# Performance work log

Measured on AMD Instinct MI355X. Metric: run time of the kernel, lower is better.

The kernel has to match this reference:

```python
import jax, jax.numpy as jnp
import numpy as np

BUFFER_SIZE = 64  # chunk size == sliding window size


def setup_inputs() -> dict:
    key = jax.random.key(0)
    k1, k2, k3, k4 = jax.random.split(key, 4)
    B, S, dim = 4, 8192, 256
    D = dim * 2
    states = jax.random.normal(k1, (B, S, dim, 2), dtype=jnp.float32)
    # projection weights (module inits them to identity; use scaled random for a
    # non-trivial but numerically tame reference)
    Wq = jax.random.normal(k2, (D, D), dtype=jnp.float32) * 0.05
    Wk = jax.random.normal(k3, (D, D), dtype=jnp.float32) * 0.05
    Wv = jax.random.normal(k4, (D, D), dtype=jnp.float32) * 0.05
    return {"states": states, "Wq": Wq, "Wk": Wk, "Wv": Wv}


def reference(states, Wq, Wk, Wv):
    B, S, dim, _ = states.shape
    D = dim * 2
    C = BUFFER_SIZE
    assert S % C == 0 and S > 2 * C
    n = S // C  # number of chunks

    x = states.reshape(B, S, D)
    q = x @ Wq.T
    k = x @ Wk.T
    v = x @ Wv.T

    # chunk: [B, n, C, D]
    qc = q.reshape(B, n, C, D)
    kc = k.reshape(B, n, C, D)
    vc = v.reshape(B, n, C, D)

    # context for chunk i = chunk i-1 ++ chunk i  -> [B, n, 2C, D]
    zeros_blk = jnp.zeros_like(kc[:, :1])
    k_ctx = jnp.concatenate([jnp.concatenate([zeros_blk, kc[:, :-1]], axis=1), kc], axis=2)
    v_ctx = jnp.concatenate([jnp.concatenate([zeros_blk, vc[:, :-1]], axis=1), vc], axis=2)

    scale = 1.0 / jnp.sqrt(jnp.asarray(D, dtype=q.dtype))
    scores = jnp.einsum('bnqd,bnkd->bnqk', qc, k_ctx) * scale  # [B, n, C, 2C]

    # mask: query at local pos qi attends keys strictly before it (global),
    # i.e. context index j < C + qi; chunk 0 has no previous chunk (j >= C).
    qi = jnp.arange(C)[:, None]            # [C,1]
    j = jnp.arange(2 * C)[None, :]         # [1,2C]
    chunk_idx = jnp.arange(n)[:, None, None]
    mask = (j < C + qi)[None] & ((chunk_idx > 0) | (j >= C)[None])  # [n, C, 2C]

    scores = jnp.where(mask[None], scores, jnp.asarray(-1e30, scores.dtype))
    p = jax.nn.softmax(scores, axis=-1)
    # fully-masked rows (only global position 0) -> zero output
    row_valid = jnp.any(mask, axis=-1, keepdims=True)[None].astype(p.dtype)
    p = p * row_valid

    out = jnp.einsum('bnqk,bnkd->bnqd', p, v_ctx).reshape(B, S, D)
    out = out.at[:, 0, :].set(0.0)  # matches retrieved_flat[:, 0, :] = 0.0
    return out.reshape(B, S, dim, 2)
```

## Files before the change

kernel.cpp:

```cpp
#include <hip/hip_runtime.h>

#define SCALE 0.044194173824159216f

typedef _Float16 half8 __attribute__((ext_vector_type(8)));
typedef _Float16 half4 __attribute__((ext_vector_type(4)));
typedef float    f32x4 __attribute__((ext_vector_type(4)));

#define MFMA(A, B, Cc) __builtin_amdgcn_mfma_f32_16x16x32_f16((A), (B), (Cc), 0, 0, 0)

#define X16_OFF 0ull
#define Q16_OFF 33554432ull
#define K16_OFF 67108864ull
#define VT_OFF  100663296ull
#define W16_OFF 134217728ull
#define WS_NEED 135790592ull

typedef __attribute__((address_space(1))) const unsigned int glb_t;
typedef __attribute__((address_space(3))) unsigned int lds_t;

__device__ __forceinline__ void gl16(const void* g, void* l) {
  __builtin_amdgcn_global_load_lds((glb_t*)g, (lds_t*)l, 16, 0, 0);
}

__device__ __forceinline__ half8 ldf64(const _Float16* buf, int row, int colh) {
  int byte = row * 128 + (((colh) << 1) ^ ((row & 7) << 4));
  return *(const half8*)((const char*)buf + byte);
}
__device__ __forceinline__ half8 ldf128(const _Float16* buf, int row, int colh) {
  int byte = row * 256 + (((colh) << 1) ^ ((row & 7) << 4));
  return *(const half8*)((const char*)buf + byte);
}

__global__ __launch_bounds__(256)
void k0_cvt(const float* __restrict__ x, const float* __restrict__ Wq,
            const float* __restrict__ Wk, const float* __restrict__ Wv,
            _Float16* __restrict__ x16, _Float16* __restrict__ w16)
{
  const long long NX = 16777216LL;
  long long base = ((long long)blockIdx.x * 256 + threadIdx.x) * 8;
  const float* src;
  _Float16* dst;
  float sc = 1.0f;
  if (base < NX) {
    src = x + base; dst = x16 + base;
  } else {
    long long o = base - NX;
    int ws = (int)(o >> 18);
    long long oo = o & 262143LL;
    src = (ws == 0 ? Wq : (ws == 1 ? Wk : Wv)) + oo;
    dst = w16 + o;
    if (ws == 0) sc = SCALE;
  }
  const float4* p = (const float4*)src;
  float4 f0 = p[0], f1 = p[1];
  half8 v;
  v[0] = (_Float16)(f0.x * sc); v[1] = (_Float16)(f0.y * sc);
  v[2] = (_Float16)(f0.z * sc); v[3] = (_Float16)(f0.w * sc);
  v[4] = (_Float16)(f1.x * sc); v[5] = (_Float16)(f1.y * sc);
  v[6] = (_Float16)(f1.z * sc); v[7] = (_Float16)(f1.w * sc);
  *(half8*)dst = v;
}

__global__ __launch_bounds__(256)
void k1_gemm(const _Float16* __restrict__ x16, const _Float16* __restrict__ w16,
             _Float16* __restrict__ q16, _Float16* __restrict__ k16,
             _Float16* __restrict__ vT)
{
  __shared__ _Float16 xs[2][8192];
  __shared__ _Float16 wl[2][8192];

  const int id  = blockIdx.x;
  const int swz = (id & 7) * 384 + (id >> 3);
  const int ntile = swz % 12;
  const int stile = swz / 12;
  const int wsel  = ntile >> 2;
  const int tid = threadIdx.x, lane = tid & 63, w = tid >> 6;
  const int l15 = lane & 15, h = lane >> 4;
  const int wm = w >> 1, wn = w & 1;

  const _Float16* xb = x16 + (size_t)stile * 128 * 512;
  const _Float16* wb = w16 + (size_t)ntile * 128 * 512;

  int rowi[4], coli[4];
  #pragma unroll
  for (int i = 0; i < 4; ++i) {
    int unit = i * 256 + w * 64 + lane;
    int row = unit >> 3, u = unit & 7;
    rowi[i] = row;
    coli[i] = (u ^ (row & 7)) << 3;
  }

  f32x4 acc[4][4] = {};
  const bool vpath = (wsel == 2);

  #pragma unroll
  for (int i = 0; i < 4; ++i) {
    int ub = i * 256 + w * 64;
    gl16(xb + (size_t)rowi[i] * 512 + coli[i], &xs[0][ub * 8]);
    gl16(wb + (size_t)rowi[i] * 512 + coli[i], &wl[0][ub * 8]);
  }

  for (int kk = 0; kk < 8; ++kk) {
    const int cur = kk & 1;
    if (kk < 7) {
      const int nxt = cur ^ 1;
      #pragma unroll
      for (int i = 0; i < 4; ++i) {
        int ub = i * 256 + w * 64;
        gl16(xb + (size_t)rowi[i] * 512 + (kk + 1) * 64 + coli[i], &xs[nxt][ub * 8]);
        gl16(wb + (size_t)rowi[i] * 512 + (kk + 1) * 64 + coli[i], &wl[nxt][ub * 8]);
      }
      asm volatile("s_waitcnt vmcnt(8)" ::: "memory");
    } else {
      asm volatile("s_waitcnt vmcnt(0)" ::: "memory");
    }
    __builtin_amdgcn_s_barrier();
    __builtin_amdgcn_sched_barrier(0);

    #pragma unroll
    for (int ks = 0; ks < 2; ++ks) {
      half8 a[4], bf[4];
      if (!vpath) {
        #pragma unroll
        for (int mr = 0; mr < 4; ++mr) a[mr]  = ldf64(xs[cur], wm * 64 + mr * 16 + l15, ks * 32 + h * 8);
        #pragma unroll
        for (int nr = 0; nr < 4; ++nr) bf[nr] = ldf64(wl[cur], wn * 64 + nr * 16 + l15, ks * 32 + h * 8);
      } else {
        #pragma unroll
        for (int mr = 0; mr < 4; ++mr) a[mr]  = ldf64(wl[cur], wm * 64 + mr * 16 + l15, ks * 32 + h * 8);
        #pragma unroll
        for (int nr = 0; nr < 4; ++nr) bf[nr] = ldf64(xs[cur], wn * 64 + nr * 16 + l15, ks * 32 + h * 8);
      }
      #pragma unroll
      for (int mr = 0; mr < 4; ++mr)
        #pragma unroll
        for (int nr = 0; nr < 4; ++nr)
          acc[mr][nr] = MFMA(a[mr], bf[nr], acc[mr][nr]);
    }

    __builtin_amdgcn_sched_barrier(0);
    __builtin_amdgcn_s_barrier();
  }

  if (!vpath) {
    _Float16* dst = (wsel == 0) ? q16 : k16;
    const int m0 = stile * 128 + wm * 64;
    const int n0 = (ntile & 3) * 128 + wn * 64;
    #pragma unroll
    for (int mr = 0; mr < 4; ++mr)
      #pragma unroll
      for (int nr = 0; nr < 4; ++nr)
        #pragma unroll
        for (int r = 0; r < 4; ++r)
          dst[(size_t)(m0 + mr * 16 + h * 4 + r) * 512 + n0 + nr * 16 + l15] =
              (_Float16)acc[mr][nr][r];
  } else {
    const int d0 = (ntile & 3) * 128 + wm * 64;
    const int sg = stile * 128 + wn * 64;
    const int bb = sg >> 13, s0 = sg & 8191;
    _Float16* dst = vT + (size_t)bb * 512 * 8192;
    #pragma unroll
    for (int mr = 0; mr < 4; ++mr)
      #pragma unroll
      for (int nr = 0; nr < 4; ++nr)
        #pragma unroll
        for (int r = 0; r < 4; ++r)
          dst[(size_t)(d0 + mr * 16 + h * 4 + r) * 8192 + s0 + nr * 16 + l15] =
              (_Float16)acc[mr][nr][r];
  }
}

__global__ __launch_bounds__(256)
void k2_attn(const _Float16* __restrict__ q16, const _Float16* __restrict__ k16,
             const _Float16* __restrict__ vT, float* __restrict__ out)
{
  __shared__ _Float16 kj[2][128 * 64];
  __shared__ _Float16 p_lds[64 * 128];

  const int id = blockIdx.x;
  const int sz = (id & 7) * 64 + (id >> 3);
  const int b = sz >> 7, c = sz & 127;
  const int tid = threadIdx.x, lane = tid & 63, w = tid >> 6;
  const int l15 = lane & 15, h = lane >> 4;
  const int jbase = c * 64 - 64;

  const _Float16* qrow = q16 + (size_t)(b * 8192 + c * 64 + w * 16 + l15) * 512;
  half8 qa[16];
  #pragma unroll
  for (int ks = 0; ks < 16; ++ks) qa[ks] = *(const half8*)(qrow + ks * 32 + h * 8);

  const _Float16* kb = k16 + (size_t)b * 8192 * 512;

  f32x4 S[8] = {};
  {
    #pragma unroll
    for (int i = 0; i < 4; ++i) {
      int unit = i * 256 + w * 64 + lane;
      int row = unit >> 3, u = unit & 7;
      int sj = jbase + row; if (sj < 0) sj = 0;
      gl16(kb + (size_t)sj * 512 + ((u ^ (row & 7)) << 3), &kj[0][(i * 256 + w * 64) * 8]);
    }
    int cur = 0;
    for (int ee = 0; ee < 8; ++ee) {
      __syncthreads();
      if (ee < 7) {
        #pragma unroll
        for (int i = 0; i < 4; ++i) {
          int unit = i * 256 + w * 64 + lane;
          int row = unit >> 3, u = unit & 7;
          int sj = jbase + row; if (sj < 0) sj = 0;
          gl16(kb + (size_t)sj * 512 + (ee + 1) * 64 + ((u ^ (row & 7)) << 3),
               &kj[cur ^ 1][(i * 256 + w * 64) * 8]);
        }
      }
      #pragma unroll
      for (int ks = 0; ks < 2; ++ks) {
        #pragma unroll
        for (int nt = 0; nt < 8; ++nt) {
          half8 bf = ldf64(kj[cur], nt * 16 + l15, ks * 32 + h * 8);
          S[nt] = MFMA(qa[ee * 2 + ks], bf, S[nt]);
        }
      }
      cur ^= 1;
    }
  }

  #pragma unroll
  for (int jt = 0; jt < 8; ++jt) {
    int j = jt * 16 + l15;
    #pragma unroll
    for (int r = 0; r < 4; ++r) {
      int ql = w * 16 + h * 4 + r;
      bool valid = (j < 64 + ql) && ((c > 0) || (j >= 64));
      S[jt][r] = valid ? S[jt][r] : -1e30f;
    }
  }
  #pragma unroll
  for (int r = 0; r < 4; ++r) {
    float mx = -1e30f;
    #pragma unroll
    for (int jt = 0; jt < 8; ++jt) mx = fmaxf(mx, S[jt][r]);
    mx = fmaxf(mx, __shfl_xor(mx, 1));
    mx = fmaxf(mx, __shfl_xor(mx, 2));
    mx = fmaxf(mx, __shfl_xor(mx, 4));
    mx = fmaxf(mx, __shfl_xor(mx, 8));
    float sum = 0.f;
    #pragma unroll
    for (int jt = 0; jt < 8; ++jt) {
      float sv = S[jt][r];
      float pe = (sv > -1e29f) ? __expf(sv - mx) : 0.f;
      S[jt][r] = pe;
      sum += pe;
    }
    sum += __shfl_xor(sum, 1);
    sum += __shfl_xor(sum, 2);
    sum += __shfl_xor(sum, 4);
    sum += __shfl_xor(sum, 8);
    float inv = (sum > 0.f) ? (1.0f / sum) : 0.f;
    #pragma unroll
    for (int jt = 0; jt < 8; ++jt) {
      int row = w * 16 + h * 4 + r, col = jt * 16 + l15;
      _Float16 ph = (_Float16)(S[jt][r] * inv);
      *(_Float16*)((char*)p_lds + row * 256 + ((col << 1) ^ ((row & 7) << 4))) = ph;
    }
  }
  half8 pa[4];
  #pragma unroll
  for (int ks = 0; ks < 4; ++ks) {
    int row = w * 16 + l15, colh = ks * 32 + h * 8;
    pa[ks] = *(const half8*)((const char*)p_lds + row * 256 + ((colh << 1) ^ ((row & 7) << 4)));
  }

  const _Float16* vb = vT + (size_t)b * 512 * 8192;
  float* ob = out + (size_t)(b * 8192 + c * 64 + w * 16) * 512;

  __syncthreads();
  #pragma unroll
  for (int i = 0; i < 4; ++i) {
    int unit = i * 256 + w * 64 + lane;
    int row = unit >> 4, u = unit & 15;
    int u2 = (u & 8) | ((u & 7) ^ (row & 7));
    int js = jbase + u2 * 8; if (js < 0) js = 0;
    gl16(vb + (size_t)row * 8192 + js, &kj[0][(i * 256 + w * 64) * 8]);
  }
  int cur = 0;
  for (int dd = 0; dd < 8; ++dd) {
    __syncthreads();
    if (dd < 7) {
      #pragma unroll
      for (int i = 0; i < 4; ++i) {
        int unit = i * 256 + w * 64 + lane;
        int row = unit >> 4, u = unit & 15;
        int u2 = (u & 8) | ((u & 7) ^ (row & 7));
        int js = jbase + u2 * 8; if (js < 0) js = 0;
        gl16(vb + (size_t)((dd + 1) * 64 + row) * 8192 + js, &kj[cur ^ 1][(i * 256 + w * 64) * 8]);
      }
    }
    f32x4 o[4] = {};
    #pragma unroll
    for (int ks = 0; ks < 4; ++ks) {
      #pragma unroll
      for (int nr = 0; nr < 4; ++nr) {
        half8 bf = ldf128(kj[cur], nr * 16 + l15, ks * 32 + h * 8);
        o[nr] = MFMA(pa[ks], bf, o[nr]);
      }
    }
    #pragma unroll
    for (int nr = 0; nr < 4; ++nr)
      #pragma unroll
      for (int r = 0; r < 4; ++r)
        ob[(size_t)(h * 4 + r) * 512 + dd * 64 + nr * 16 + l15] = o[nr][r];
    cur ^= 1;
  }
}

__device__ __forceinline__ int swzb(int row, int colByte) {
  return colByte ^ ((row & 7) << 4);
}
__device__ __forceinline__ half8 ldw_frag(const float* __restrict__ W, int row, int e0) {
  const float4* p = reinterpret_cast<const float4*>(W + ((size_t)row << 9) + e0);
  float4 f0 = p[0];
  float4 f1 = p[1];
  half8 v;
  v[0] = (_Float16)f0.x; v[1] = (_Float16)f0.y; v[2] = (_Float16)f0.z; v[3] = (_Float16)f0.w;
  v[4] = (_Float16)f1.x; v[5] = (_Float16)f1.y; v[6] = (_Float16)f1.z; v[7] = (_Float16)f1.w;
  return v;
}
__device__ __forceinline__ half8 ldl_frag(const unsigned short* buf, int row, int col, int strideBytes) {
  int byte = row * strideBytes + swzb(row, col << 1);
  return *reinterpret_cast<const half8*>(reinterpret_cast<const char*>(buf) + byte);
}

__global__ __launch_bounds__(256, 1)
void ep_fused(const float* __restrict__ x, const float* __restrict__ Wq,
              const float* __restrict__ Wk, const float* __restrict__ Wv,
              float* __restrict__ out)
{
  __shared__ unsigned short xs[128 * 512];
  __shared__ unsigned short kv[64 * 128];
  __shared__ unsigned short pq[64 * 128];

  const int bc   = blockIdx.x;
  const int b    = bc >> 7;
  const int c    = bc & 127;
  const int tid  = threadIdx.x;
  const int lane = tid & 63;
  const int w    = tid >> 6;
  const int l15  = lane & 15;
  const int h    = lane >> 4;

  const float* xb = x + (size_t)b * (8192 * 512);
  #pragma unroll
  for (int i = 0; i < 32; ++i) {
    int unit = tid + (i << 8);
    int row  = unit >> 6;
    int e0   = (unit & 63) << 3;
    half8 v;
    if (c == 0 && row < 64) {
      #pragma unroll
      for (int t = 0; t < 8; ++t) v[t] = (_Float16)0.0f;
    } else {
      int s = c * 64 - 64 + row;
      const float4* p = reinterpret_cast<const float4*>(xb + (size_t)s * 512 + e0);
      float4 f0 = p[0], f1 = p[1];
      v[0] = (_Float16)f0.x; v[1] = (_Float16)f0.y; v[2] = (_Float16)f0.z; v[3] = (_Float16)f0.w;
      v[4] = (_Float16)f1.x; v[5] = (_Float16)f1.y; v[6] = (_Float16)f1.z; v[7] = (_Float16)f1.w;
    }
    int byte = (row << 10) + swzb(row, e0 << 1);
    *reinterpret_cast<half8*>(reinterpret_cast<char*>(xs) + byte) = v;
  }
  __syncthreads();

  f32x4 Sacc[8] = {};
  const int d0 = (w << 4) + (h << 2);

  for (int dt = 0; dt < 8; ++dt) {
    const int drow = (dt << 6) + (w << 4) + l15;

    f32x4 qa[4] = {};
    for (int ks = 0; ks < 16; ++ks) {
      half8 a = ldw_frag(Wq, drow, (ks << 5) + (h << 3));
      #pragma unroll
      for (int nt = 0; nt < 4; ++nt) {
        half8 bf = ldl_frag(xs, 64 + (nt << 4) + l15, (ks << 5) + (h << 3), 1024);
        qa[nt] = MFMA(a, bf, qa[nt]);
      }
    }
    #pragma unroll
    for (int nt = 0; nt < 4; ++nt) {
      int q = (nt << 4) + l15;
      half4 hv;
      hv[0] = (_Float16)qa[nt][0]; hv[1] = (_Float16)qa[nt][1];
      hv[2] = (_Float16)qa[nt][2]; hv[3] = (_Float16)qa[nt][3];
      *reinterpret_cast<half4*>(reinterpret_cast<char*>(pq) + q * 128 + swzb(q, d0 << 1)) = hv;
    }

    f32x4 ka[8] = {};
    for (int ks = 0; ks < 16; ++ks) {
      half8 a = ldw_frag(Wk, drow, (ks << 5) + (h << 3));
      #pragma unroll
      for (int nt = 0; nt < 8; ++nt) {
        half8 bf = ldl_frag(xs, (nt << 4) + l15, (ks << 5) + (h << 3), 1024);
        ka[nt] = MFMA(a, bf, ka[nt]);
      }
    }
    #pragma unroll
    for (int nt = 0; nt < 8; ++nt) {
      int j = (nt << 4) + l15;
      half4 hv;
      hv[0] = (_Float16)ka[nt][0]; hv[1] = (_Float16)ka[nt][1];
      hv[2] = (_Float16)ka[nt][2]; hv[3] = (_Float16)ka[nt][3];
      *reinterpret_cast<half4*>(reinterpret_cast<char*>(kv) + j * 128 + swzb(j, d0 << 1)) = hv;
    }
    __syncthreads();

    #pragma unroll
    for (int ksd = 0; ksd < 2; ++ksd) {
      half8 a = ldl_frag(pq, (w << 4) + l15, (ksd << 5) + (h << 3), 128);
      #pragma unroll
      for (int nt = 0; nt < 8; ++nt) {
        half8 bf = ldl_frag(kv, (nt << 4) + l15, (ksd << 5) + (h << 3), 128);
        Sacc[nt] = MFMA(a, bf, Sacc[nt]);
      }
    }
    __syncthreads();
  }

  const float scale = SCALE;
  #pragma unroll
  for (int nt = 0; nt < 8; ++nt) {
    int j = (nt << 4) + l15;
    #pragma unroll
    for (int r = 0; r < 4; ++r) {
      int qrow = (w << 4) + (h << 2) + r;
      bool valid = (j < 64 + qrow) && ((c > 0) || (j >= 64));
      Sacc[nt][r] = valid ? Sacc[nt][r] * scale : -1e30f;
    }
  }
  float inv[4];
  #pragma unroll
  for (int r = 0; r < 4; ++r) {
    float mx = -1e30f;
    #pragma unroll
    for (int nt = 0; nt < 8; ++nt) mx = fmaxf(mx, Sacc[nt][r]);
    mx = fmaxf(mx, __shfl_xor(mx, 1));
    mx = fmaxf(mx, __shfl_xor(mx, 2));
    mx = fmaxf(mx, __shfl_xor(mx, 4));
    mx = fmaxf(mx, __shfl_xor(mx, 8));
    float sum = 0.f;
    #pragma unroll
    for (int nt = 0; nt < 8; ++nt) {
      float sv = Sacc[nt][r];
      float pe = (sv > -1e29f) ? __expf(sv - mx) : 0.f;
      Sacc[nt][r] = pe;
      sum += pe;
    }
    sum += __shfl_xor(sum, 1);
    sum += __shfl_xor(sum, 2);
    sum += __shfl_xor(sum, 4);
    sum += __shfl_xor(sum, 8);
    inv[r] = (sum > 0.f) ? (1.0f / sum) : 0.f;
  }
  #pragma unroll
  for (int nt = 0; nt < 8; ++nt) {
    int j = (nt << 4) + l15;
    #pragma unroll
    for (int r = 0; r < 4; ++r) {
      int qrow = (w << 4) + (h << 2) + r;
      _Float16 ph = (_Float16)(Sacc[nt][r] * inv[r]);
      *reinterpret_cast<_Float16*>(reinterpret_cast<char*>(pq) + qrow * 256 + swzb(qrow, j << 1)) = ph;
    }
  }
  __syncthreads();

  for (int dt = 0; dt < 8; ++dt) {
    const int dcol = (dt << 6) + (w << 4) + l15;

    f32x4 va[8] = {};
    for (int ks = 0; ks < 16; ++ks) {
      half8 bf = ldw_frag(Wv, dcol, (ks << 5) + (h << 3));
      #pragma unroll
      for (int mt = 0; mt < 8; ++mt) {
        half8 a = ldl_frag(xs, (mt << 4) + l15, (ks << 5) + (h << 3), 1024);
        va[mt] = MFMA(a, bf, va[mt]);
      }
    }
    {
      int dl = (w << 4) + l15;
      #pragma unroll
      for (int mt = 0; mt < 8; ++mt) {
        int j0 = (mt << 4) + (h << 2);
        half4 hv;
        hv[0] = (_Float16)va[mt][0]; hv[1] = (_Float16)va[mt][1];
        hv[2] = (_Float16)va[mt][2]; hv[3] = (_Float16)va[mt][3];
        *reinterpret_cast<half4*>(reinterpret_cast<char*>(kv) + dl * 256 + swzb(dl, j0 << 1)) = hv;
      }
    }
    __syncthreads();

    f32x4 oa[4] = {};
    #pragma unroll
    for (int ks = 0; ks < 4; ++ks) {
      half8 a = ldl_frag(pq, (w << 4) + l15, (ks << 5) + (h << 3), 256);
      #pragma unroll
      for (int nt = 0; nt < 4; ++nt) {
        half8 bf = ldl_frag(kv, (nt << 4) + l15, (ks << 5) + (h << 3), 256);
        oa[nt] = MFMA(a, bf, oa[nt]);
      }
    }
    #pragma unroll
    for (int nt = 0; nt < 4; ++nt) {
      int d = (dt << 6) + (nt << 4) + l15;
      #pragma unroll
      for (int r = 0; r < 4; ++r) {
        int qrow = (w << 4) + (h << 2) + r;
        out[((size_t)(b * 8192 + (c << 6) + qrow) << 9) + d] = oa[nt][r];
      }
    }
    __syncthreads();
  }
}

extern "C" void kernel_launch(void* const* d_in, const int* in_sizes, int n_in,
                              void* d_out, int out_size, void* d_ws, size_t ws_size,
                              hipStream_t stream) {
  const float* x  = (const float*)d_in[0];
  const float* Wq = (const float*)d_in[1];
  const float* Wk = (const float*)d_in[2];
  const float* Wv = (const float*)d_in[3];
  float* out = (float*)d_out;
  (void)in_sizes; (void)n_in; (void)out_size;

  if (d_ws != nullptr && ws_size >= WS_NEED) {
    char* ws = (char*)d_ws;
    _Float16* x16 = (_Float16*)(ws + X16_OFF);
    _Float16* q16 = (_Float16*)(ws + Q16_OFF);
    _Float16* k16 = (_Float16*)(ws + K16_OFF);
    _Float16* vT  = (_Float16*)(ws + VT_OFF);
    _Float16* w16 = (_Float16*)(ws + W16_OFF);

    hipLaunchKernelGGL(k0_cvt, dim3(8576), dim3(256), 0, stream, x, Wq, Wk, Wv, x16, w16);
    hipLaunchKernelGGL(k1_gemm, dim3(3072), dim3(256), 0, stream, x16, w16, q16, k16, vT);
    hipLaunchKernelGGL(k2_attn, dim3(512), dim3(256), 0, stream, q16, k16, vT, out);
  } else {
    hipLaunchKernelGGL(ep_fused, dim3(512), dim3(256), 0, stream, x, Wq, Wk, Wv, out);
  }
}
```

Baseline: 113.4 us.

## Enlarge QKV projection GEMM tiles to 256x256 with interleaved 4-phase pipeline

The projection GEMM now uses 256x256 output tiles with 512 threads (8 waves, each computing 128x64), 64 KB double-buffered LDS, and a four-phase schedule. Each phase issues part of the next K-slice's global-to-LDS loads, then runs an MFMA quarter at raised wave priority. The larger tile is meant to cut global and LDS traffic per FLOP and to overlap loads with compute more finely. In exchange it uses more registers and LDS per block and launches far fewer blocks (768 instead of 3072), which may reduce occupancy and tail balance.

```diff
diff --git a/kernel.cpp b/kernel.cpp
--- a/kernel.cpp
+++ b/kernel.cpp
@@ -61,112 +61,176 @@
   *(half8*)dst = v;
 }
 
-__global__ __launch_bounds__(256)
+__global__ __launch_bounds__(512, 2)
 void k1_gemm(const _Float16* __restrict__ x16, const _Float16* __restrict__ w16,
              _Float16* __restrict__ q16, _Float16* __restrict__ k16,
              _Float16* __restrict__ vT)
 {
-  __shared__ _Float16 xs[2][8192];
-  __shared__ _Float16 wl[2][8192];
+  __shared__ _Float16 As[2][16384];
+  __shared__ _Float16 Bs[2][16384];
 
   const int id  = blockIdx.x;
-  const int swz = (id & 7) * 384 + (id >> 3);
-  const int ntile = swz % 12;
-  const int stile = swz / 12;
-  const int wsel  = ntile >> 2;
+  const int swz = (id & 7) * 96 + (id >> 3);
+  const int ntile = swz % 6;
+  const int stile = swz / 6;
+  const int wsel  = ntile >> 1;
+  const bool vpath = (wsel == 2);
+
   const int tid = threadIdx.x, lane = tid & 63, w = tid >> 6;
   const int l15 = lane & 15, h = lane >> 4;
-  const int wm = w >> 1, wn = w & 1;
-
-  const _Float16* xb = x16 + (size_t)stile * 128 * 512;
-  const _Float16* wb = w16 + (size_t)ntile * 128 * 512;
-
-  int rowi[4], coli[4];
+  const int wm = w >> 2, wn = w & 3;
+
+  const _Float16* xb = x16 + (size_t)stile * 256 * 512;
+  const _Float16* wb = w16 + (size_t)ntile * 256 * 512;
+
+  const int t6 = tid >> 3, u8 = tid & 7;
+  const int colsw = ((u8 ^ (t6 & 7)) << 3);
+  const int gA[4] = { t6, 128 + t6, 64 + t6, 192 + t6 };
+  int gB[4];
   #pragma unroll
   for (int i = 0; i < 4; ++i) {
-    int unit = i * 256 + w * 64 + lane;
-    int row = unit >> 3, u = unit & 7;
-    rowi[i] = row;
-    coli[i] = (u ^ (row & 7)) << 3;
-  }
-
-  f32x4 acc[4][4] = {};
-  const bool vpath = (wsel == 2);
-
-  #pragma unroll
-  for (int i = 0; i < 4; ++i) {
-    int ub = i * 256 + w * 64;
-    gl16(xb + (size_t)rowi[i] * 512 + coli[i], &xs[0][ub * 8]);
-    gl16(wb + (size_t)rowi[i] * 512 + coli[i], &wl[0][ub * 8]);
-  }
-
-  for (int kk = 0; kk < 8; ++kk) {
-    const int cur = kk & 1;
-    if (kk < 7) {
-      const int nxt = cur ^ 1;
-      #pragma unroll
-      for (int i = 0; i < 4; ++i) {
-        int ub = i * 256 + w * 64;
-        gl16(xb + (size_t)rowi[i] * 512 + (kk + 1) * 64 + coli[i], &xs[nxt][ub * 8]);
-        gl16(wb + (size_t)rowi[i] * 512 + (kk + 1) * 64 + coli[i], &wl[nxt][ub * 8]);
-      }
-      asm volatile("s_waitcnt vmcnt(8)" ::: "memory");
-    } else {
-      asm volatile("s_waitcnt vmcnt(0)" ::: "memory");
-    }
+    int pp = i * 64 + t6;
+    gB[i] = (((pp >> 5) & 3) << 6) + ((pp >> 7) << 5) + (pp & 31);
+  }
+
+#define STAGE_A2(par, i0, kc)                                                      \
+  { gl16(xb + (size_t)gA[i0] * 512 + (kc) + colsw, &As[par][((i0)*512 + w*64)*8]); \
+    gl16(xb + (size_t)gA[(i0)+1] * 512 + (kc) + colsw, &As[par][(((i0)+1)*512 + w*64)*8]); }
+#define STAGE_B2(par, i0, kc)                                                      \
+  { gl16(wb + (size_t)gB[i0] * 512 + (kc) + colsw, &Bs[par][((i0)*512 + w*64)*8]); \
+    gl16(wb + (size_t)gB[(i0)+1] * 512 + (kc) + colsw, &Bs[par][(((i0)+1)*512 + w*64)*8]); }
+
+  f32x4 acc[8][4] = {};
+  half8 af[8], bf0[4], bf1[4];
+
+  STAGE_A2(0, 0, 0);
+  STAGE_B2(0, 0, 0);
+  STAGE_B2(0, 2, 0);
+  STAGE_A2(0, 2, 0);
+  asm volatile("s_waitcnt vmcnt(4)" ::: "memory");
+  __builtin_amdgcn_s_barrier();
+  __builtin_amdgcn_sched_barrier(0);
+
+  for (int t = 0; t < 8; ++t) {
+    const int p = t & 1, np = p ^ 1;
+    const _Float16* Ap = As[p];
+    const _Float16* Bp = Bs[p];
+    const int kc = (t + 1) * 64;
+    const bool stg = (t < 7);
+
+    if (stg) STAGE_A2(np, 0, kc);
+    #pragma unroll
+    for (int m = 0; m < 4; ++m)
+      #pragma unroll
+      for (int ks = 0; ks < 2; ++ks)
+        af[m*2+ks] = ldf64(Ap, wm*64 + m*16 + l15, ks*32 + h*8);
+    #pragma unroll
+    for (int n = 0; n < 2; ++n)
+      #pragma unroll
+      for (int ks = 0; ks < 2; ++ks)
+        bf0[n*2+ks] = ldf64(Bp, wn*32 + n*16 + l15, ks*32 + h*8);
+    __builtin_amdgcn_s_barrier();
+    __builtin_amdgcn_s_setprio(1);
+    #pragma unroll
+    for (int m = 0; m < 4; ++m)
+      #pragma unroll
+      for (int n = 0; n < 2; ++n)
+        #pragma unroll
+        for (int ks = 0; ks < 2; ++ks)
+          acc[m][n] = vpath ? MFMA(bf0[n*2+ks], af[m*2+ks], acc[m][n])
+                            : MFMA(af[m*2+ks], bf0[n*2+ks], acc[m][n]);
+    __builtin_amdgcn_s_setprio(0);
+    if (stg) { asm volatile("s_waitcnt vmcnt(4)" ::: "memory"); }
+    else     { asm volatile("s_waitcnt vmcnt(2)" ::: "memory"); }
     __builtin_amdgcn_s_barrier();
     __builtin_amdgcn_sched_barrier(0);
 
-    #pragma unroll
-    for (int ks = 0; ks < 2; ++ks) {
-      half8 a[4], bf[4];
-      if (!vpath) {
-        #pragma unroll
-        for (int mr = 0; mr < 4; ++mr) a[mr]  = ldf64(xs[cur], wm * 64 + mr * 16 + l15, ks * 32 + h * 8);
-        #pragma unroll
-        for (int nr = 0; nr < 4; ++nr) bf[nr] = ldf64(wl[cur], wn * 64 + nr * 16 + l15, ks * 32 + h * 8);
-      } else {
-        #pragma unroll
-        for (int mr = 0; mr < 4; ++mr) a[mr]  = ldf64(wl[cur], wm * 64 + mr * 16 + l15, ks * 32 + h * 8);
-        #pragma unroll
-        for (int nr = 0; nr < 4; ++nr) bf[nr] = ldf64(xs[cur], wn * 64 + nr * 16 + l15, ks * 32 + h * 8);
-      }
-      #pragma unroll
-      for (int mr = 0; mr < 4; ++mr)
-        #pragma unroll
-        for (int nr = 0; nr < 4; ++nr)
-          acc[mr][nr] = MFMA(a[mr], bf[nr], acc[mr][nr]);
-    }
-
+    if (stg) STAGE_B2(np, 0, kc);
+    #pragma unroll
+    for (int n = 0; n < 2; ++n)
+      #pragma unroll
+      for (int ks = 0; ks < 2; ++ks)
+        bf1[n*2+ks] = ldf64(Bp, 128 + wn*32 + n*16 + l15, ks*32 + h*8);
+    __builtin_amdgcn_s_barrier();
+    __builtin_amdgcn_s_setprio(1);
+    #pragma unroll
+    for (int m = 0; m < 4; ++m)
+      #pragma unroll
+      for (int n = 0; n < 2; ++n)
+        #pragma unroll
+        for (int ks = 0; ks < 2; ++ks)
+          acc[m][2+n] = vpath ? MFMA(bf1[n*2+ks], af[m*2+ks], acc[m][2+n])
+                              : MFMA(af[m*2+ks], bf1[n*2+ks], acc[m][2+n]);
+    __builtin_amdgcn_s_setprio(0);
+    if (stg) { asm volatile("s_waitcnt vmcnt(4)" ::: "memory"); }
+    else     { asm volatile("s_waitcnt vmcnt(0)" ::: "memory"); }
+    __builtin_amdgcn_s_barrier();
     __builtin_amdgcn_sched_barrier(0);
-    __builtin_amdgcn_s_barrier();
-  }
+
+    if (stg) STAGE_B2(np, 2, kc);
+    #pragma unroll
+    for (int m = 0; m < 4; ++m)
+      #pragma unroll
+      for (int ks = 0; ks < 2; ++ks)
+        af[m*2+ks] = ldf64(Ap, 128 + wm*64 + m*16 + l15, ks*32 + h*8);
+    __builtin_amdgcn_s_barrier();
+    __builtin_amdgcn_s_setprio(1);
+    #pragma unroll
+    for (int m = 0; m < 4; ++m)
+      #pragma unroll
+      for (int n = 0; n < 2; ++n)
+        #pragma unroll
+        for (int ks = 0; ks < 2; ++ks)
+          acc[4+m][2+n] = vpath ? MFMA(bf1[n*2+ks], af[m*2+ks], acc[4+m][2+n])
+                                : MFMA(af[m*2+ks], bf1[n*2+ks], acc[4+m][2+n]);
+    __builtin_amdgcn_s_setprio(0);
+    __builtin_amdgcn_s_barrier();
+    __builtin_amdgcn_sched_barrier(0);
+
+    if (stg) STAGE_A2(np, 2, kc);
+    __builtin_amdgcn_s_barrier();
+    __builtin_amdgcn_s_setprio(1);
+    #pragma unroll
+    for (int m = 0; m < 4; ++m)
+      #pragma unroll
+      for (int n = 0; n < 2; ++n)
+        #pragma unroll
+        for (int ks = 0; ks < 2; ++ks)
+          acc[4+m][n] = vpath ? MFMA(bf0[n*2+ks], af[m*2+ks], acc[4+m][n])
+                              : MFMA(af[m*2+ks], bf0[n*2+ks], acc[4+m][n]);
+    __builtin_amdgcn_s_setprio(0);
+    if (stg) { asm volatile("s_waitcnt vmcnt(4)" ::: "memory"); }
+    __builtin_amdgcn_s_barrier();
+    __builtin_amdgcn_sched_barrier(0);
+  }
+#undef STAGE_A2
+#undef STAGE_B2
 
   if (!vpath) {
     _Float16* dst = (wsel == 0) ? q16 : k16;
-    const int m0 = stile * 128 + wm * 64;
-    const int n0 = (ntile & 3) * 128 + wn * 64;
-    #pragma unroll
-    for (int mr = 0; mr < 4; ++mr)
-      #pragma unroll
-      for (int nr = 0; nr < 4; ++nr)
+    const int m0 = stile * 256 + wm * 128;
+    const int n0 = (ntile & 1) * 256 + wn * 64;
+    #pragma unroll
+    for (int mf = 0; mf < 8; ++mf)
+      #pragma unroll
+      for (int nf = 0; nf < 4; ++nf)
         #pragma unroll
         for (int r = 0; r < 4; ++r)
-          dst[(size_t)(m0 + mr * 16 + h * 4 + r) * 512 + n0 + nr * 16 + l15] =
-              (_Float16)acc[mr][nr][r];
+          dst[(size_t)(m0 + mf * 16 + h * 4 + r) * 512 + n0 + nf * 16 + l15] =
+              (_Float16)acc[mf][nf][r];
   } else {
-    const int d0 = (ntile & 3) * 128 + wm * 64;
-    const int sg = stile * 128 + wn * 64;
+    const int d0 = (ntile & 1) * 256 + wn * 64;
+    const int sg = stile * 256 + wm * 128;
     const int bb = sg >> 13, s0 = sg & 8191;
     _Float16* dst = vT + (size_t)bb * 512 * 8192;
     #pragma unroll
-    for (int mr = 0; mr < 4; ++mr)
-      #pragma unroll
-      for (int nr = 0; nr < 4; ++nr)
+    for (int mf = 0; mf < 8; ++mf)
+      #pragma unroll
+      for (int nf = 0; nf < 4; ++nf)
         #pragma unroll
         for (int r = 0; r < 4; ++r)
-          dst[(size_t)(d0 + mr * 16 + h * 4 + r) * 8192 + s0 + nr * 16 + l15] =
-              (_Float16)acc[mr][nr][r];
+          dst[(size_t)(d0 + nf * 16 + h * 4 + r) * 8192 + s0 + mf * 16 + l15] =
+              (_Float16)acc[mf][nf][r];
   }
 }
 
@@ -540,7 +604,7 @@
     _Float16* w16 = (_Float16*)(ws + W16_OFF);
 
     hipLaunchKernelGGL(k0_cvt, dim3(8576), dim3(256), 0, stream, x, Wq, Wk, Wv, x16, w16);
-    hipLaunchKernelGGL(k1_gemm, dim3(3072), dim3(256), 0, stream, x16, w16, q16, k16, vT);
+    hipLaunchKernelGGL(k1_gemm, dim3(768), dim3(512), 0, stream, x16, w16, q16, k16, vT);
     hipLaunchKernelGGL(k2_attn, dim3(512), dim3(256), 0, stream, q16, k16, vT, out);
   } else {
     hipLaunchKernelGGL(ep_fused, dim3(512), dim3(256), 0, stream, x, Wq, Wk, Wv, out);
```

Result: slower. 138.6 us (+22.3%).

## Load projection weight fragments directly into registers instead of staging through LDS

Applied to the files above, without the earlier changes.

The QKV projection GEMM stops staging the weight tile through shared memory. Each lane now loads its weight MFMA fragments straight from global memory into a double-buffered register array, while the activation tile still goes through LDS via global_load_lds. This halves LDS use and LDS read traffic per block, at the cost of extra VGPRs and uncoalesced 16-byte global loads for the weights, which may rely on L2 for reuse. The outer k-loop is fully unrolled and the vmcnt wait count is adjusted to match.

```diff
diff --git a/kernel.cpp b/kernel.cpp
--- a/kernel.cpp
+++ b/kernel.cpp
@@ -67,13 +67,13 @@
              _Float16* __restrict__ vT)
 {
   __shared__ _Float16 xs[2][8192];
-  __shared__ _Float16 wl[2][8192];
 
   const int id  = blockIdx.x;
   const int swz = (id & 7) * 384 + (id >> 3);
   const int ntile = swz % 12;
   const int stile = swz / 12;
   const int wsel  = ntile >> 2;
+  const bool vpath = (wsel == 2);
   const int tid = threadIdx.x, lane = tid & 63, w = tid >> 6;
   const int l15 = lane & 15, h = lane >> 4;
   const int wm = w >> 1, wn = w & 1;
@@ -84,33 +84,46 @@
   int rowi[4], coli[4];
   #pragma unroll
   for (int i = 0; i < 4; ++i) {
-    int unit = i * 256 + w * 64 + lane;
+    int unit = i * 256 + tid;
     int row = unit >> 3, u = unit & 7;
     rowi[i] = row;
     coli[i] = (u ^ (row & 7)) << 3;
   }
 
+  const int wrb = (vpath ? wm : wn) * 64;
+  const int xrb = (vpath ? wn : wm) * 64;
+  const _Float16* wrow[4];
+  #pragma unroll
+  for (int f = 0; f < 4; ++f)
+    wrow[f] = wb + (size_t)(wrb + f * 16 + l15) * 512 + h * 8;
+
   f32x4 acc[4][4] = {};
-  const bool vpath = (wsel == 2);
-
-  #pragma unroll
-  for (int i = 0; i < 4; ++i) {
-    int ub = i * 256 + w * 64;
-    gl16(xb + (size_t)rowi[i] * 512 + coli[i], &xs[0][ub * 8]);
-    gl16(wb + (size_t)rowi[i] * 512 + coli[i], &wl[0][ub * 8]);
-  }
-
+  half8 wf[2][8];
+
+  #pragma unroll
+  for (int i = 0; i < 4; ++i)
+    gl16(xb + (size_t)rowi[i] * 512 + coli[i], &xs[0][(i * 256 + w * 64) * 8]);
+  #pragma unroll
+  for (int f = 0; f < 4; ++f)
+    #pragma unroll
+    for (int ks = 0; ks < 2; ++ks)
+      wf[0][f * 2 + ks] = *(const half8*)(wrow[f] + ks * 32);
+
+  #pragma unroll
   for (int kk = 0; kk < 8; ++kk) {
-    const int cur = kk & 1;
+    const int cur = kk & 1, nxt = cur ^ 1;
     if (kk < 7) {
-      const int nxt = cur ^ 1;
-      #pragma unroll
-      for (int i = 0; i < 4; ++i) {
-        int ub = i * 256 + w * 64;
-        gl16(xb + (size_t)rowi[i] * 512 + (kk + 1) * 64 + coli[i], &xs[nxt][ub * 8]);
-        gl16(wb + (size_t)rowi[i] * 512 + (kk + 1) * 64 + coli[i], &wl[nxt][ub * 8]);
-      }
-      asm volatile("s_waitcnt vmcnt(8)" ::: "memory");
+      #pragma unroll
+      for (int i = 0; i < 4; ++i)
+        gl16(xb + (size_t)rowi[i] * 512 + (kk + 1) * 64 + coli[i],
+             &xs[nxt][(i * 256 + w * 64) * 8]);
+      #pragma unroll
+      for (int f = 0; f < 4; ++f)
+        #pragma unroll
+        for (int ks = 0; ks < 2; ++ks)
+          wf[nxt][f * 2 + ks] = *(const half8*)(wrow[f] + (kk + 1) * 64 + ks * 32);
+      __builtin_amdgcn_sched_barrier(0);
+      asm volatile("s_waitcnt vmcnt(12)" ::: "memory");
     } else {
       asm volatile("s_waitcnt vmcnt(0)" ::: "memory");
     }
@@ -119,23 +132,16 @@
 
     #pragma unroll
     for (int ks = 0; ks < 2; ++ks) {
-      half8 a[4], bf[4];
-      if (!vpath) {
-        #pragma unroll
-        for (int mr = 0; mr < 4; ++mr) a[mr]  = ldf64(xs[cur], wm * 64 + mr * 16 + l15, ks * 32 + h * 8);
-        #pragma unroll
-        for (int nr = 0; nr < 4; ++nr) bf[nr] = ldf64(wl[cur], wn * 64 + nr * 16 + l15, ks * 32 + h * 8);
-      } else {
-        #pragma unroll
-        for (int mr = 0; mr < 4; ++mr) a[mr]  = ldf64(wl[cur], wm * 64 + mr * 16 + l15, ks * 32 + h * 8);
-        #pragma unroll
-        for (int nr = 0; nr < 4; ++nr) bf[nr] = ldf64(xs[cur], wn * 64 + nr * 16 + l15, ks * 32 + h * 8);
-      }
+      half8 xf[4];
+      #pragma unroll
+      for (int f = 0; f < 4; ++f)
+        xf[f] = ldf64(xs[cur], xrb + f * 16 + l15, ks * 32 + h * 8);
       #pragma unroll
       for (int mr = 0; mr < 4; ++mr)
         #pragma unroll
         for (int nr = 0; nr < 4; ++nr)
-          acc[mr][nr] = MFMA(a[mr], bf[nr], acc[mr][nr]);
+          acc[mr][nr] = vpath ? MFMA(wf[cur][mr * 2 + ks], xf[nr], acc[mr][nr])
+                              : MFMA(xf[mr], wf[cur][nr * 2 + ks], acc[mr][nr]);
     }
 
     __builtin_amdgcn_sched_barrier(0);
```

New measurement: 171.2 us. 51.0% more time.

## Fold Wq and Wk into one matrix so attention scores use raw x as keys

Applied to the files above, without the earlier changes.

Scores are rewritten as (x·Wqᵀ)(x·Wkᵀ)ᵀ = x·(WqᵀWk)·xᵀ. A small kernel now precomputes M = scale·Wkᵀ·Wq in fp16, and the GEMM kernel produces y = x·M and V only, dropping from 12 to 8 column tiles and from 3072 to 2048 blocks. The attention kernel then uses y as queries and the fp16 x itself as keys, so the separate K projection is no longer computed or written. It adds an extra naive fp32 kernel launch of 256 blocks and changes rounding, because the product M is stored in fp16.

```diff
diff --git a/kernel.cpp b/kernel.cpp
--- a/kernel.cpp
+++ b/kernel.cpp
@@ -9,8 +9,8 @@
 #define MFMA(A, B, Cc) __builtin_amdgcn_mfma_f32_16x16x32_f16((A), (B), (Cc), 0, 0, 0)
 
 #define X16_OFF 0ull
-#define Q16_OFF 33554432ull
-#define K16_OFF 67108864ull
+#define Y16_OFF 33554432ull
+#define MT_OFF  67108864ull
 #define VT_OFF  100663296ull
 #define W16_OFF 134217728ull
 #define WS_NEED 135790592ull
@@ -62,24 +62,45 @@
 }
 
 __global__ __launch_bounds__(256)
+void kmm(const float* __restrict__ Wq, const float* __restrict__ Wk,
+         _Float16* __restrict__ Mt)
+{
+  const int t = threadIdx.x, blk = blockIdx.x;
+  const int g0 = (blk >> 5) * 64 + (t >> 4) * 4;
+  const int e  = (blk & 31) * 16 + (t & 15);
+  float a0 = 0.f, a1 = 0.f, a2 = 0.f, a3 = 0.f;
+  #pragma unroll 8
+  for (int f = 0; f < 512; ++f) {
+    float4 kv = *(const float4*)(Wk + (size_t)f * 512 + g0);
+    float  qv = Wq[(size_t)f * 512 + e];
+    a0 += kv.x * qv; a1 += kv.y * qv; a2 += kv.z * qv; a3 += kv.w * qv;
+  }
+  Mt[(size_t)(g0 + 0) * 512 + e] = (_Float16)(a0 * SCALE);
+  Mt[(size_t)(g0 + 1) * 512 + e] = (_Float16)(a1 * SCALE);
+  Mt[(size_t)(g0 + 2) * 512 + e] = (_Float16)(a2 * SCALE);
+  Mt[(size_t)(g0 + 3) * 512 + e] = (_Float16)(a3 * SCALE);
+}
+
+__global__ __launch_bounds__(256)
 void k1_gemm(const _Float16* __restrict__ x16, const _Float16* __restrict__ w16,
-             _Float16* __restrict__ q16, _Float16* __restrict__ k16,
+             const _Float16* __restrict__ Mt, _Float16* __restrict__ y16,
              _Float16* __restrict__ vT)
 {
   __shared__ _Float16 xs[2][8192];
   __shared__ _Float16 wl[2][8192];
 
   const int id  = blockIdx.x;
-  const int swz = (id & 7) * 384 + (id >> 3);
-  const int ntile = swz % 12;
-  const int stile = swz / 12;
-  const int wsel  = ntile >> 2;
+  const int swz = (id & 7) * 256 + (id >> 3);
+  const int ntile = swz & 7;
+  const int stile = swz >> 3;
+  const bool vpath = (ntile >= 4);
   const int tid = threadIdx.x, lane = tid & 63, w = tid >> 6;
   const int l15 = lane & 15, h = lane >> 4;
   const int wm = w >> 1, wn = w & 1;
 
   const _Float16* xb = x16 + (size_t)stile * 128 * 512;
-  const _Float16* wb = w16 + (size_t)ntile * 128 * 512;
+  const _Float16* wb = vpath ? w16 + (size_t)(1024 + (ntile & 3) * 128) * 512
+                             : Mt  + (size_t)((ntile & 3) * 128) * 512;
 
   int rowi[4], coli[4];
   #pragma unroll
@@ -91,7 +112,6 @@
   }
 
   f32x4 acc[4][4] = {};
-  const bool vpath = (wsel == 2);
 
   #pragma unroll
   for (int i = 0; i < 4; ++i) {
@@ -143,7 +163,6 @@
   }
 
   if (!vpath) {
-    _Float16* dst = (wsel == 0) ? q16 : k16;
     const int m0 = stile * 128 + wm * 64;
     const int n0 = (ntile & 3) * 128 + wn * 64;
     #pragma unroll
@@ -152,7 +171,7 @@
       for (int nr = 0; nr < 4; ++nr)
         #pragma unroll
         for (int r = 0; r < 4; ++r)
-          dst[(size_t)(m0 + mr * 16 + h * 4 + r) * 512 + n0 + nr * 16 + l15] =
+          y16[(size_t)(m0 + mr * 16 + h * 4 + r) * 512 + n0 + nr * 16 + l15] =
               (_Float16)acc[mr][nr][r];
   } else {
     const int d0 = (ntile & 3) * 128 + wm * 64;
@@ -171,7 +190,7 @@
 }
 
 __global__ __launch_bounds__(256)
-void k2_attn(const _Float16* __restrict__ q16, const _Float16* __restrict__ k16,
+void k2_attn(const _Float16* __restrict__ y16, const _Float16* __restrict__ x16,
              const _Float16* __restrict__ vT, float* __restrict__ out)
 {
   __shared__ _Float16 kj[2][128 * 64];
@@ -184,12 +203,12 @@
   const int l15 = lane & 15, h = lane >> 4;
   const int jbase = c * 64 - 64;
 
-  const _Float16* qrow = q16 + (size_t)(b * 8192 + c * 64 + w * 16 + l15) * 512;
+  const _Float16* qrow = y16 + (size_t)(b * 8192 + c * 64 + w * 16 + l15) * 512;
   half8 qa[16];
   #pragma unroll
   for (int ks = 0; ks < 16; ++ks) qa[ks] = *(const half8*)(qrow + ks * 32 + h * 8);
 
-  const _Float16* kb = k16 + (size_t)b * 8192 * 512;
+  const _Float16* kb = x16 + (size_t)b * 8192 * 512;
 
   f32x4 S[8] = {};
   {
@@ -534,14 +553,15 @@
   if (d_ws != nullptr && ws_size >= WS_NEED) {
     char* ws = (char*)d_ws;
     _Float16* x16 = (_Float16*)(ws + X16_OFF);
-    _Float16* q16 = (_Float16*)(ws + Q16_OFF);
-    _Float16* k16 = (_Float16*)(ws + K16_OFF);
+    _Float16* y16 = (_Float16*)(ws + Y16_OFF);
+    _Float16* Mt  = (_Float16*)(ws + MT_OFF);
     _Float16* vT  = (_Float16*)(ws + VT_OFF);
     _Float16* w16 = (_Float16*)(ws + W16_OFF);
 
     hipLaunchKernelGGL(k0_cvt, dim3(8576), dim3(256), 0, stream, x, Wq, Wk, Wv, x16, w16);
-    hipLaunchKernelGGL(k1_gemm, dim3(3072), dim3(256), 0, stream, x16, w16, q16, k16, vT);
-    hipLaunchKernelGGL(k2_attn, dim3(512), dim3(256), 0, stream, q16, k16, vT, out);
+    hipLaunchKernelGGL(kmm, dim3(256), dim3(256), 0, stream, Wq, Wk, Mt);
+    hipLaunchKernelGGL(k1_gemm, dim3(2048), dim3(256), 0, stream, x16, w16, Mt, y16, vT);
+    hipLaunchKernelGGL(k2_attn, dim3(512), dim3(256), 0, stream, y16, x16, vT, out);
   } else {
     hipLaunchKernelGGL(ep_fused, dim3(512), dim3(256), 0, stream, x, Wq, Wk, Wv, out);
   }
```

Result: slower. 131.4 us (+15.9%).
